# Performance work log

Measured on AMD Instinct MI355X. Metric: run time of the kernel, lower is better.

The kernel has to match this reference:

```python
import jax, jax.numpy as jnp
import numpy as np

B, F, D, H, E, K = 4, 2048, 1024, 2048, 8, 2  # batch, frames, dim, expert hidden, n_experts, top_k


def setup_inputs() -> dict:
    key = jax.random.key(0)
    ks = jax.random.split(key, 9)
    sc = lambda k, shape, fan_in: (jax.random.normal(k, shape, jnp.float32) * (fan_in ** -0.5))
    return {
        "x": jax.random.normal(ks[0], (B, F, D), jnp.float32),
        # router: Linear(D,D) -> SiLU -> Linear(D,E)
        "rw1": sc(ks[1], (D, D), D),
        "rb1": jnp.zeros((D,), jnp.float32),
        "rw2": sc(ks[2], (D, E), D),
        "rb2": jnp.zeros((E,), jnp.float32),
        # experts: E x (Linear(D,H) -> SiLU -> Linear(H,D))
        "ew1": sc(ks[3], (E, D, H), D),
        "eb1": jnp.zeros((E, H), jnp.float32),
        "ew2": sc(ks[4], (E, H, D), H),
        "eb2": jnp.zeros((E, D), jnp.float32),
    }


def reference(x, rw1, rb1, rw2, rb2, ew1, eb1, ew2, eb2):
    b, f, d = x.shape
    t = x.reshape(b * f, d)                                   # [T, D]
    # router (eval mode: no topk noise)
    logits = jax.nn.silu(t @ rw1 + rb1) @ rw2 + rb2            # [T, E]
    vals, idx = jax.lax.top_k(logits, K)                       # [T, K]
    rows = jnp.arange(t.shape[0])[:, None]
    masked = jnp.full_like(logits, -jnp.inf).at[rows, idx].set(vals)
    w = jax.nn.softmax(masked, axis=1)                         # [T, E], nonzero only on top-k
    # dense per-expert FFN, then weighted combine (residual: y starts as x)
    eh = jax.nn.silu(jnp.einsum('td,edh->teh', t, ew1) + eb1[None])   # [T, E, H]
    eo = jnp.einsum('teh,ehd->ted', eh, ew2) + eb2[None]              # [T, E, D]
    y = t + jnp.einsum('te,ted->td', w, eo)
    return y.reshape(b, f, d)
```

## Files before the change

kernel.cpp:

```cpp
#include <hip/hip_runtime.h>
#include <hip/hip_bf16.h>
#include <cstdint>
#include <cstddef>

#define T_TOK 8192
#define DDIM  1024
#define HDIM  2048
#define NEXP  8
#define TOPK  2
#define KAUG  (3 * DDIM)

typedef short bf16x8 __attribute__((ext_vector_type(8)));
typedef float f32x4  __attribute__((ext_vector_type(4)));

__device__ __forceinline__ unsigned short f2bf(float f) {
  union { float f; unsigned u; } v; v.f = f;
  unsigned r = v.u + 0x7FFFu + ((v.u >> 16) & 1u);
  return (unsigned short)(r >> 16);
}
__device__ __forceinline__ float bf2f(unsigned short h) {
  union { unsigned u; float f; } v; v.u = ((unsigned)h) << 16;
  return v.f;
}
__device__ __forceinline__ float silu_fast(float v) {
  return v / (1.0f + __expf(-v));
}
__device__ __forceinline__ float silu_precise(float v) {
  return v / (1.0f + expf(-v));
}

__device__ __forceinline__ void gload16(const unsigned short* g, unsigned short* l) {
  __builtin_amdgcn_global_load_lds(
      (const __attribute__((address_space(1))) unsigned int*)g,
      (__attribute__((address_space(3))) unsigned int*)l,
      16, 0, 0);
}

__global__ void split_x_kernel(const float* __restrict__ in,
                               unsigned short* __restrict__ xaug, int n4) {
  int i = blockIdx.x * blockDim.x + threadIdx.x;
  if (i >= n4) return;
  float4 v = ((const float4*)in)[i];
  int t = i / (DDIM / 4);
  int kc = (i % (DDIM / 4)) * 4;
  float f[4] = {v.x, v.y, v.z, v.w};
  ushort4 hi, lo;
  unsigned short h[4], l[4];
#pragma unroll
  for (int j = 0; j < 4; j++) {
    h[j] = f2bf(f[j]);
    l[j] = f2bf(f[j] - bf2f(h[j]));
  }
  hi.x = h[0]; hi.y = h[1]; hi.z = h[2]; hi.w = h[3];
  lo.x = l[0]; lo.y = l[1]; lo.z = l[2]; lo.w = l[3];
  *(ushort4*)&xaug[(size_t)t * KAUG + kc] = hi;
  *(ushort4*)&xaug[(size_t)t * KAUG + DDIM + kc] = hi;
  *(ushort4*)&xaug[(size_t)t * KAUG + 2 * DDIM + kc] = lo;
}

__global__ __launch_bounds__(256) void split_w_kernel(
    const float* __restrict__ in, unsigned short* __restrict__ waug) {
  __shared__ float tile[32][33];
  int c0 = blockIdx.x * 32, r0 = blockIdx.y * 32;
  int tx = threadIdx.x & 31, ty = threadIdx.x >> 5;
#pragma unroll
  for (int i = 0; i < 32; i += 8)
    tile[ty + i][tx] = in[(size_t)(r0 + ty + i) * DDIM + (c0 + tx)];
  __syncthreads();
#pragma unroll
  for (int i = 0; i < 32; i += 8) {
    float v = tile[tx][ty + i];
    unsigned short h = f2bf(v);
    unsigned short l = f2bf(v - bf2f(h));
    int n = c0 + ty + i, k = r0 + tx;
    waug[(size_t)n * KAUG + k] = h;
    waug[(size_t)n * KAUG + DDIM + k] = l;
    waug[(size_t)n * KAUG + 2 * DDIM + k] = h;
  }
}

__global__ __launch_bounds__(256) void transpose_conv_kernel(
    const float* __restrict__ in, unsigned short* __restrict__ out, int R, int C) {
  __shared__ float tile[32][33];
  const int z = blockIdx.z;
  const float* src = in + (size_t)z * R * C;
  unsigned short* dst = out + (size_t)z * R * C;
  int c0 = blockIdx.x * 32, r0 = blockIdx.y * 32;
  int tx = threadIdx.x & 31, ty = threadIdx.x >> 5;
#pragma unroll
  for (int i = 0; i < 32; i += 8)
    tile[ty + i][tx] = src[(size_t)(r0 + ty + i) * C + (c0 + tx)];
  __syncthreads();
#pragma unroll
  for (int i = 0; i < 32; i += 8)
    dst[(size_t)(c0 + ty + i) * R + (r0 + tx)] = f2bf(tile[tx][ty + i]);
}

__global__ void zero_small_kernel(int* __restrict__ counts, int* __restrict__ cursors) {
  int i = threadIdx.x;
  if (i < NEXP) { counts[i] = 0; cursors[i] = 0; }
}

template <int EPI, int BNT>
__global__ __launch_bounds__(512, 2) void gemm_mfma2(
    const unsigned short* __restrict__ Abase,
    const unsigned short* __restrict__ Btbase,
    const float* __restrict__ bias,
    float* __restrict__ outF,
    unsigned short* __restrict__ outBf,
    const int* __restrict__ toks,
    const int* __restrict__ offs, const int* __restrict__ cnts,
    int N, int KD, int Astride, int numE, int nTiles, int mCap) {
  constexpr int NI = BNT / 64;
  constexpr int RB = BNT / 64;
  constexpr int BB = BNT * 128;
  extern __shared__ char sm[];

  const int id = blockIdx.x;
  const int e = id % numE;
  const int r = id / numE;
  const int n0 = (r % nTiles) * BNT;
  const int mb = r / nTiles;

  int ne = T_TOK, off = 0;
  if (EPI != 0) { ne = cnts[e]; off = offs[e]; }

  const unsigned short* Bt = Btbase + (size_t)e * N * KD;
  const unsigned short* A = (EPI == 2) ? (Abase + (size_t)off * Astride) : Abase;

  const int tid = threadIdx.x;
  const int lane = tid & 63, wid = tid >> 6;
  const int l16 = lane & 15, quad = lane >> 4;
  const int wm = wid >> 2, wn = wid & 3;

  const int rStage = tid >> 3;
  const int cS8 = ((tid & 7) ^ (rStage & 7)) * 8;
  const int ldsW = wid << 10;

  const int NT = KD / 64;
  const int mStride = mCap * 256;

  const int sw = l16 & 7;
  const int cOff0 = (quad ^ sw) << 4;
  const int cOff1 = ((quad + 4) ^ sw) << 4;
  const int aRowB = (wm * 128 + l16) << 7;
  const int bRowB = (wn * (NI * 16) + l16) << 7;

  const unsigned short* bPtr[RB];
#pragma unroll
  for (int p = 0; p < RB; p++)
    bPtr[p] = Bt + (size_t)(n0 + p * 64 + rStage) * KD + cS8;

  for (int m0 = mb * 256; m0 < ne; m0 += mStride) {
    const unsigned short* aPtr[4];
#pragma unroll
    for (int p = 0; p < 4; p++) {
      int row = m0 + p * 64 + rStage;
      int idx;
      if (EPI == 1) idx = toks[off + min(row, ne - 1)];
      else if (EPI == 2) idx = min(row, ne - 1);
      else idx = row;
      aPtr[p] = A + (size_t)idx * Astride + cS8;
    }

    f32x4 acc[8][NI];
    const f32x4 zf = {0.f, 0.f, 0.f, 0.f};
#pragma unroll
    for (int mi = 0; mi < 8; mi++)
#pragma unroll
      for (int ni = 0; ni < NI; ni++) acc[mi][ni] = zf;

#pragma unroll
    for (int p = 0; p < 4; p++)
      gload16(aPtr[p], (unsigned short*)(sm + p * 8192 + ldsW));
#pragma unroll
    for (int p = 0; p < RB; p++)
      gload16(bPtr[p], (unsigned short*)(sm + 65536 + p * 8192 + ldsW));
    __builtin_amdgcn_s_waitcnt(0x0F70);
    __builtin_amdgcn_s_barrier();
    __builtin_amdgcn_sched_barrier(0);

    int cur = 0;
    for (int t = 0; t < NT; ++t) {
      const int nxt = cur ^ 1;
      const bool pf = (t + 1) < NT;
      const int kb = (t + 1) * 64;
      const char* cbA = sm + cur * 32768;
      const char* cbB = sm + 65536 + cur * BB;

      if (pf) {
#pragma unroll
        for (int p = 0; p < 4; p++)
          gload16(aPtr[p] + kb, (unsigned short*)(sm + nxt * 32768 + p * 8192 + ldsW));
      }
      bf16x8 av[8], bv[NI];
#pragma unroll
      for (int mi = 0; mi < 8; mi++)
        av[mi] = *(const bf16x8*)(cbA + aRowB + (mi << 11) + cOff0);
#pragma unroll
      for (int ni = 0; ni < NI; ni++)
        bv[ni] = *(const bf16x8*)(cbB + bRowB + (ni << 11) + cOff0);
      __builtin_amdgcn_s_barrier();
      __builtin_amdgcn_s_setprio(1);
#pragma unroll
      for (int mi = 0; mi < 8; mi++)
#pragma unroll
        for (int ni = 0; ni < NI; ni++)
          acc[mi][ni] = __builtin_amdgcn_mfma_f32_16x16x32_bf16(
              av[mi], bv[ni], acc[mi][ni], 0, 0, 0);
      __builtin_amdgcn_s_setprio(0);

      if (pf) {
#pragma unroll
        for (int p = 0; p < RB; p++)
          gload16(bPtr[p] + kb,
                  (unsigned short*)(sm + 65536 + nxt * BB + p * 8192 + ldsW));
      }
#pragma unroll
      for (int mi = 0; mi < 8; mi++)
        av[mi] = *(const bf16x8*)(cbA + aRowB + (mi << 11) + cOff1);
#pragma unroll
      for (int ni = 0; ni < NI; ni++)
        bv[ni] = *(const bf16x8*)(cbB + bRowB + (ni << 11) + cOff1);
      __builtin_amdgcn_s_setprio(1);
#pragma unroll
      for (int mi = 0; mi < 8; mi++)
#pragma unroll
        for (int ni = 0; ni < NI; ni++)
          acc[mi][ni] = __builtin_amdgcn_mfma_f32_16x16x32_bf16(
              av[mi], bv[ni], acc[mi][ni], 0, 0, 0);
      __builtin_amdgcn_s_setprio(0);
      __builtin_amdgcn_s_waitcnt(0x0F70);
      __builtin_amdgcn_s_barrier();
      __builtin_amdgcn_sched_barrier(0);
      cur = nxt;
    }

    float bv4[NI];
#pragma unroll
    for (int ni = 0; ni < NI; ni++)
      bv4[ni] = bias[(size_t)e * N + n0 + wn * (NI * 16) + ni * 16 + l16];
#pragma unroll
    for (int mi = 0; mi < 8; mi++) {
      const int prow = m0 + wm * 128 + mi * 16 + quad * 4;
#pragma unroll
      for (int rr = 0; rr < 4; rr++) {
        const int p = prow + rr;
        if (EPI != 0 && p >= ne) continue;
#pragma unroll
        for (int ni = 0; ni < NI; ni++) {
          const int col = n0 + wn * (NI * 16) + ni * 16 + l16;
          float v = acc[mi][ni][rr] + bv4[ni];
          if (EPI == 0) {
            outF[(size_t)p * N + col] = silu_precise(v);
          } else if (EPI == 1) {
            outBf[(size_t)(off + p) * N + col] = f2bf(silu_fast(v));
          } else {
            outBf[(size_t)(off + p) * N + col] = f2bf(v);
          }
        }
      }
    }
  }
}

__global__ __launch_bounds__(256) void router2_kernel(
    const float* __restrict__ rh, const float* __restrict__ rw2,
    const float* __restrict__ rb2, float* __restrict__ logits) {
  int t = blockIdx.x * 4 + (threadIdx.x >> 6);
  int lane = threadIdx.x & 63;
  const float* row = rh + (size_t)t * DDIM;
  float acc[NEXP];
#pragma unroll
  for (int e = 0; e < NEXP; e++) acc[e] = 0.f;
  for (int k = lane; k < DDIM; k += 64) {
    float v = row[k];
    const float* w = rw2 + (size_t)k * NEXP;
#pragma unroll
    for (int e = 0; e < NEXP; e++) acc[e] += v * w[e];
  }
#pragma unroll
  for (int e = 0; e < NEXP; e++) {
#pragma unroll
    for (int off = 32; off > 0; off >>= 1) acc[e] += __shfl_xor(acc[e], off, 64);
  }
#pragma unroll
  for (int e = 0; e < NEXP; e++)
    if (lane == e) logits[(size_t)t * NEXP + e] = acc[e] + rb2[e];
}

__global__ void topk_kernel(const float* __restrict__ logits,
                            int* __restrict__ idx2, float* __restrict__ w2arr,
                            int* __restrict__ counts) {
  int t = blockIdx.x * blockDim.x + threadIdx.x;
  if (t >= T_TOK) return;
  float l[NEXP];
#pragma unroll
  for (int e = 0; e < NEXP; e++) l[e] = logits[(size_t)t * NEXP + e];
  int i1 = 0; float v1 = l[0];
#pragma unroll
  for (int e = 1; e < NEXP; e++)
    if (l[e] > v1) { v1 = l[e]; i1 = e; }
  int i2 = -1; float v2 = -3.4e38f;
#pragma unroll
  for (int e = 0; e < NEXP; e++)
    if (e != i1 && l[e] > v2) { v2 = l[e]; i2 = e; }
  float ex = expf(v2 - v1);
  float wa = 1.f / (1.f + ex);
  float wb = ex / (1.f + ex);
  idx2[t * 2] = i1; idx2[t * 2 + 1] = i2;
  w2arr[t * 2] = wa; w2arr[t * 2 + 1] = wb;
  atomicAdd(&counts[i1], 1);
  atomicAdd(&counts[i2], 1);
}

__global__ void prefix_kernel(const int* __restrict__ counts, int* __restrict__ offs) {
  if (threadIdx.x == 0 && blockIdx.x == 0) {
    int s = 0;
    for (int e = 0; e < NEXP; e++) { offs[e] = s; s += counts[e]; }
  }
}

__global__ void scatter_kernel(const int* __restrict__ idx2,
                               const int* __restrict__ offs, int* __restrict__ cursors,
                               int* __restrict__ toks, int* __restrict__ posArr) {
  int t = blockIdx.x * blockDim.x + threadIdx.x;
  if (t >= T_TOK) return;
#pragma unroll
  for (int j = 0; j < TOPK; j++) {
    int e = idx2[t * 2 + j];
    int pos = atomicAdd(&cursors[e], 1);
    int s = offs[e] + pos;
    toks[s] = t;
    posArr[t * 2 + j] = s;
  }
}

__global__ __launch_bounds__(256) void combine_kernel(
    const float* __restrict__ x, const unsigned short* __restrict__ eo,
    const int* __restrict__ posArr, const float* __restrict__ w2arr,
    float* __restrict__ y) {
  const int t = blockIdx.x;
  const int d = threadIdx.x * 4;
  const int s0 = posArr[t * 2], s1 = posArr[t * 2 + 1];
  const float w0 = w2arr[t * 2], w1 = w2arr[t * 2 + 1];
  float4 xv = *(const float4*)&x[(size_t)t * DDIM + d];
  ushort4 a = *(const ushort4*)&eo[(size_t)s0 * DDIM + d];
  ushort4 b = *(const ushort4*)&eo[(size_t)s1 * DDIM + d];
  float4 o;
  o.x = xv.x + w0 * bf2f(a.x) + w1 * bf2f(b.x);
  o.y = xv.y + w0 * bf2f(a.y) + w1 * bf2f(b.y);
  o.z = xv.z + w0 * bf2f(a.z) + w1 * bf2f(b.z);
  o.w = xv.w + w0 * bf2f(a.w) + w1 * bf2f(b.w);
  *(float4*)&y[(size_t)t * DDIM + d] = o;
}

extern "C" void kernel_launch(void* const* d_in, const int* in_sizes, int n_in,
                              void* d_out, int out_size, void* d_ws, size_t ws_size,
                              hipStream_t stream) {
  (void)in_sizes; (void)n_in; (void)out_size; (void)ws_size;
  const float* x   = (const float*)d_in[0];
  const float* rw1 = (const float*)d_in[1];
  const float* rb1 = (const float*)d_in[2];
  const float* rw2 = (const float*)d_in[3];
  const float* rb2 = (const float*)d_in[4];
  const float* ew1 = (const float*)d_in[5];
  const float* eb1 = (const float*)d_in[6];
  const float* ew2 = (const float*)d_in[7];
  const float* eb2 = (const float*)d_in[8];
  float* y = (float*)d_out;

  char* ws = (char*)d_ws;
  size_t o = 0;
  auto alloc = [&](size_t bytes) {
    size_t r = o;
    o += (bytes + 255) & ~(size_t)255;
    return r;
  };
  unsigned short* xaug  = (unsigned short*)(ws + alloc((size_t)T_TOK * KAUG * 2));
  unsigned short* waug  = (unsigned short*)(ws + alloc((size_t)DDIM * KAUG * 2));
  unsigned short* ew1t  = (unsigned short*)(ws + alloc((size_t)NEXP * HDIM * DDIM * 2));
  unsigned short* ew2t  = (unsigned short*)(ws + alloc((size_t)NEXP * DDIM * HDIM * 2));
  float*          rh    = (float*)(ws + alloc((size_t)T_TOK * DDIM * 4));
  float*          logits= (float*)(ws + alloc((size_t)T_TOK * NEXP * 4));
  int*            idx2  = (int*)(ws + alloc((size_t)T_TOK * 2 * 4));
  float*          w2    = (float*)(ws + alloc((size_t)T_TOK * 2 * 4));
  int*            toks  = (int*)(ws + alloc((size_t)T_TOK * TOPK * 4));
  int*            posArr= (int*)(ws + alloc((size_t)T_TOK * TOPK * 4));
  int*            counts= (int*)(ws + alloc(256));
  int*            cursors=(int*)(ws + alloc(256));
  int*            offs  = (int*)(ws + alloc(256));
  unsigned short* ehb   = (unsigned short*)(ws + alloc((size_t)T_TOK * TOPK * HDIM * 2));
  unsigned short* eo    = (unsigned short*)(ws + alloc((size_t)T_TOK * TOPK * DDIM * 2));

  constexpr int LDS_R = 98304;
  constexpr int LDS_E = 131072;
  static bool s_attr = false;
  if (!s_attr) {
    hipFuncSetAttribute((const void*)gemm_mfma2<0, 128>,
                        hipFuncAttributeMaxDynamicSharedMemorySize, LDS_R);
    hipFuncSetAttribute((const void*)gemm_mfma2<1, 256>,
                        hipFuncAttributeMaxDynamicSharedMemorySize, LDS_E);
    hipFuncSetAttribute((const void*)gemm_mfma2<2, 256>,
                        hipFuncAttributeMaxDynamicSharedMemorySize, LDS_E);
    s_attr = true;
  }

  zero_small_kernel<<<1, 64, 0, stream>>>(counts, cursors);

  const int n4 = T_TOK * DDIM / 4;
  split_x_kernel<<<(n4 + 255) / 256, 256, 0, stream>>>(x, xaug, n4);
  split_w_kernel<<<dim3(DDIM / 32, DDIM / 32), 256, 0, stream>>>(rw1, waug);
  transpose_conv_kernel<<<dim3(HDIM / 32, DDIM / 32, NEXP), 256, 0, stream>>>(ew1, ew1t, DDIM, HDIM);
  transpose_conv_kernel<<<dim3(DDIM / 32, HDIM / 32, NEXP), 256, 0, stream>>>(ew2, ew2t, HDIM, DDIM);

  gemm_mfma2<0, 128><<<256, 512, LDS_R, stream>>>(
      xaug, waug, rb1, rh, nullptr, nullptr, nullptr, nullptr,
      DDIM, KAUG, KAUG, 1, 8, 32);
  router2_kernel<<<T_TOK / 4, 256, 0, stream>>>(rh, rw2, rb2, logits);
  topk_kernel<<<T_TOK / 256, 256, 0, stream>>>(logits, idx2, w2, counts);
  prefix_kernel<<<1, 64, 0, stream>>>(counts, offs);
  scatter_kernel<<<T_TOK / 256, 256, 0, stream>>>(idx2, offs, cursors, toks, posArr);

  gemm_mfma2<1, 256><<<8 * 8 * 16, 512, LDS_E, stream>>>(
      xaug, ew1t, eb1, nullptr, ehb, toks, offs, counts,
      HDIM, DDIM, KAUG, NEXP, 8, 16);
  gemm_mfma2<2, 256><<<8 * 4 * 16, 512, LDS_E, stream>>>(
      ehb, ew2t, eb2, nullptr, eo, nullptr, offs, counts,
      DDIM, HDIM, HDIM, NEXP, 4, 16);
  combine_kernel<<<T_TOK, 256, 0, stream>>>(x, eo, posArr, w2, y);
}
```

Measured before the change: 721.1 us.

## Switch MFMA GEMM to four-stage K=32 LDS pipeline with single barrier per step

Replaces the double-buffered K=64 tile loop with a four-buffer ring of K=32 slices, keeping three slices in flight and using counted vmcnt waits so only one barrier is needed per step. The XOR swizzle of LDS columns is dropped in favour of a plain 64-byte row layout. The goal is to hide global-load latency more deeply and remove the mid-iteration barrier. The risks are LDS bank conflicts from the unswizzled layout, twice as many loop iterations with less MFMA work each, and LDS use of 128 KB per block for the expert GEMMs, which may limit occupancy.

```diff
diff --git a/kernel.cpp b/kernel.cpp
--- a/kernel.cpp
+++ b/kernel.cpp
@@ -102,7 +102,7 @@
 }
 
 template <int EPI, int BNT>
-__global__ __launch_bounds__(512, 2) void gemm_mfma2(
+__global__ __launch_bounds__(512, 2) void gemm_mfma3(
     const unsigned short* __restrict__ Abase,
     const unsigned short* __restrict__ Btbase,
     const float* __restrict__ bias,
@@ -112,8 +112,9 @@
     const int* __restrict__ offs, const int* __restrict__ cnts,
     int N, int KD, int Astride, int numE, int nTiles, int mCap) {
   constexpr int NI = BNT / 64;
-  constexpr int RB = BNT / 64;
-  constexpr int BB = BNT * 128;
+  constexpr int RB = BNT / 128;
+  constexpr int LPT = 2 + RB;
+  constexpr int BUFB = 16384 + BNT * 64;
   extern __shared__ char sm[];
 
   const int id = blockIdx.x;
@@ -133,34 +134,31 @@
   const int l16 = lane & 15, quad = lane >> 4;
   const int wm = wid >> 2, wn = wid & 3;
 
-  const int rStage = tid >> 3;
-  const int cS8 = ((tid & 7) ^ (rStage & 7)) * 8;
+  const int rStage = tid >> 2;
+  const int cS = (tid & 3) * 8;
   const int ldsW = wid << 10;
 
-  const int NT = KD / 64;
+  const int NT = KD / 32;
   const int mStride = mCap * 256;
 
-  const int sw = l16 & 7;
-  const int cOff0 = (quad ^ sw) << 4;
-  const int cOff1 = ((quad + 4) ^ sw) << 4;
-  const int aRowB = (wm * 128 + l16) << 7;
-  const int bRowB = (wn * (NI * 16) + l16) << 7;
-
-  const unsigned short* bPtr[RB];
+  const int aFragB = ((wm * 128 + l16) << 6) + (quad << 4);
+  const int bFragB = 16384 + ((wn * (NI * 16) + l16) << 6) + (quad << 4);
+
+  const unsigned short* bP[RB];
 #pragma unroll
   for (int p = 0; p < RB; p++)
-    bPtr[p] = Bt + (size_t)(n0 + p * 64 + rStage) * KD + cS8;
+    bP[p] = Bt + (size_t)(n0 + p * 128 + rStage) * KD + cS;
 
   for (int m0 = mb * 256; m0 < ne; m0 += mStride) {
-    const unsigned short* aPtr[4];
-#pragma unroll
-    for (int p = 0; p < 4; p++) {
-      int row = m0 + p * 64 + rStage;
+    const unsigned short* aP[2];
+#pragma unroll
+    for (int p = 0; p < 2; p++) {
+      int row = m0 + p * 128 + rStage;
       int idx;
       if (EPI == 1) idx = toks[off + min(row, ne - 1)];
       else if (EPI == 2) idx = min(row, ne - 1);
       else idx = row;
-      aPtr[p] = A + (size_t)idx * Astride + cS8;
+      aP[p] = A + (size_t)idx * Astride + cS;
     }
 
     f32x4 acc[8][NI];
@@ -170,37 +168,38 @@
 #pragma unroll
       for (int ni = 0; ni < NI; ni++) acc[mi][ni] = zf;
 
-#pragma unroll
-    for (int p = 0; p < 4; p++)
-      gload16(aPtr[p], (unsigned short*)(sm + p * 8192 + ldsW));
-#pragma unroll
-    for (int p = 0; p < RB; p++)
-      gload16(bPtr[p], (unsigned short*)(sm + 65536 + p * 8192 + ldsW));
-    __builtin_amdgcn_s_waitcnt(0x0F70);
-    __builtin_amdgcn_s_barrier();
-    __builtin_amdgcn_sched_barrier(0);
-
-    int cur = 0;
+    auto stage = [&](int t, int b) {
+      char* base = sm + b * BUFB + ldsW;
+#pragma unroll
+      for (int p = 0; p < 2; p++)
+        gload16(aP[p] + t * 32, (unsigned short*)(base + p * 8192));
+#pragma unroll
+      for (int p = 0; p < RB; p++)
+        gload16(bP[p] + t * 32, (unsigned short*)(base + 16384 + p * 8192));
+    };
+
+    stage(0, 0);
+    stage(1, 1);
+    stage(2, 2);
+
     for (int t = 0; t < NT; ++t) {
-      const int nxt = cur ^ 1;
-      const bool pf = (t + 1) < NT;
-      const int kb = (t + 1) * 64;
-      const char* cbA = sm + cur * 32768;
-      const char* cbB = sm + 65536 + cur * BB;
-
-      if (pf) {
-#pragma unroll
-        for (int p = 0; p < 4; p++)
-          gload16(aPtr[p] + kb, (unsigned short*)(sm + nxt * 32768 + p * 8192 + ldsW));
-      }
+      if (t + 2 < NT)      __builtin_amdgcn_s_waitcnt(0x0F70 | (2 * LPT));
+      else if (t + 1 < NT) __builtin_amdgcn_s_waitcnt(0x0F70 | LPT);
+      else                 __builtin_amdgcn_s_waitcnt(0x0F70);
+      __builtin_amdgcn_s_barrier();
+      __builtin_amdgcn_sched_barrier(0);
+
+      if (t + 3 < NT) stage(t + 3, (t + 3) & 3);
+
+      const char* base = sm + (t & 3) * BUFB;
       bf16x8 av[8], bv[NI];
 #pragma unroll
       for (int mi = 0; mi < 8; mi++)
-        av[mi] = *(const bf16x8*)(cbA + aRowB + (mi << 11) + cOff0);
+        av[mi] = *(const bf16x8*)(base + aFragB + (mi << 10));
 #pragma unroll
       for (int ni = 0; ni < NI; ni++)
-        bv[ni] = *(const bf16x8*)(cbB + bRowB + (ni << 11) + cOff0);
-      __builtin_amdgcn_s_barrier();
+        bv[ni] = *(const bf16x8*)(base + bFragB + (ni << 10));
+
       __builtin_amdgcn_s_setprio(1);
 #pragma unroll
       for (int mi = 0; mi < 8; mi++)
@@ -209,31 +208,6 @@
           acc[mi][ni] = __builtin_amdgcn_mfma_f32_16x16x32_bf16(
               av[mi], bv[ni], acc[mi][ni], 0, 0, 0);
       __builtin_amdgcn_s_setprio(0);
-
-      if (pf) {
-#pragma unroll
-        for (int p = 0; p < RB; p++)
-          gload16(bPtr[p] + kb,
-                  (unsigned short*)(sm + 65536 + nxt * BB + p * 8192 + ldsW));
-      }
-#pragma unroll
-      for (int mi = 0; mi < 8; mi++)
-        av[mi] = *(const bf16x8*)(cbA + aRowB + (mi << 11) + cOff1);
-#pragma unroll
-      for (int ni = 0; ni < NI; ni++)
-        bv[ni] = *(const bf16x8*)(cbB + bRowB + (ni << 11) + cOff1);
-      __builtin_amdgcn_s_setprio(1);
-#pragma unroll
-      for (int mi = 0; mi < 8; mi++)
-#pragma unroll
-        for (int ni = 0; ni < NI; ni++)
-          acc[mi][ni] = __builtin_amdgcn_mfma_f32_16x16x32_bf16(
-              av[mi], bv[ni], acc[mi][ni], 0, 0, 0);
-      __builtin_amdgcn_s_setprio(0);
-      __builtin_amdgcn_s_waitcnt(0x0F70);
-      __builtin_amdgcn_s_barrier();
-      __builtin_amdgcn_sched_barrier(0);
-      cur = nxt;
     }
 
     float bv4[NI];
@@ -393,15 +367,15 @@
   unsigned short* ehb   = (unsigned short*)(ws + alloc((size_t)T_TOK * TOPK * HDIM * 2));
   unsigned short* eo    = (unsigned short*)(ws + alloc((size_t)T_TOK * TOPK * DDIM * 2));
 
-  constexpr int LDS_R = 98304;
-  constexpr int LDS_E = 131072;
+  constexpr int LDS_R = 4 * (16384 + 128 * 64);
+  constexpr int LDS_E = 4 * (16384 + 256 * 64);
   static bool s_attr = false;
   if (!s_attr) {
-    hipFuncSetAttribute((const void*)gemm_mfma2<0, 128>,
+    hipFuncSetAttribute((const void*)gemm_mfma3<0, 128>,
                         hipFuncAttributeMaxDynamicSharedMemorySize, LDS_R);
-    hipFuncSetAttribute((const void*)gemm_mfma2<1, 256>,
+    hipFuncSetAttribute((const void*)gemm_mfma3<1, 256>,
                         hipFuncAttributeMaxDynamicSharedMemorySize, LDS_E);
-    hipFuncSetAttribute((const void*)gemm_mfma2<2, 256>,
+    hipFuncSetAttribute((const void*)gemm_mfma3<2, 256>,
                         hipFuncAttributeMaxDynamicSharedMemorySize, LDS_E);
     s_attr = true;
   }
@@ -414,7 +388,7 @@
   transpose_conv_kernel<<<dim3(HDIM / 32, DDIM / 32, NEXP), 256, 0, stream>>>(ew1, ew1t, DDIM, HDIM);
   transpose_conv_kernel<<<dim3(DDIM / 32, HDIM / 32, NEXP), 256, 0, stream>>>(ew2, ew2t, HDIM, DDIM);
 
-  gemm_mfma2<0, 128><<<256, 512, LDS_R, stream>>>(
+  gemm_mfma3<0, 128><<<256, 512, LDS_R, stream>>>(
       xaug, waug, rb1, rh, nullptr, nullptr, nullptr, nullptr,
       DDIM, KAUG, KAUG, 1, 8, 32);
   router2_kernel<<<T_TOK / 4, 256, 0, stream>>>(rh, rw2, rb2, logits);
@@ -422,10 +396,10 @@
   prefix_kernel<<<1, 64, 0, stream>>>(counts, offs);
   scatter_kernel<<<T_TOK / 256, 256, 0, stream>>>(idx2, offs, cursors, toks, posArr);
 
-  gemm_mfma2<1, 256><<<8 * 8 * 16, 512, LDS_E, stream>>>(
+  gemm_mfma3<1, 256><<<8 * 8 * 16, 512, LDS_E, stream>>>(
       xaug, ew1t, eb1, nullptr, ehb, toks, offs, counts,
       HDIM, DDIM, KAUG, NEXP, 8, 16);
-  gemm_mfma2<2, 256><<<8 * 4 * 16, 512, LDS_E, stream>>>(
+  gemm_mfma3<2, 256><<<8 * 4 * 16, 512, LDS_E, stream>>>(
       ehb, ew2t, eb2, nullptr, eo, nullptr, offs, counts,
       DDIM, HDIM, HDIM, NEXP, 4, 16);
   combine_kernel<<<T_TOK, 256, 0, stream>>>(x, eo, posArr, w2, y);
```

Result: slower. 739.6 us (+2.6%).
